# Optimization experiments

Hardware: AMD Instinct MI355X
Metric: run time of the kernel (lower is better)

The kernel has to match this reference:

```python
import math
import jax, jax.numpy as jnp
import numpy as np

B, S, DIM = 1, 2048, 2880
N_HEADS, N_KV, HD = 64, 8, 64
ROPE_FACTOR = 32.0
THETA = 150000.0
NEG_INF = -1e30


def setup_inputs() -> dict:
    key = jax.random.key(0)
    ks = jax.random.split(key, 12)
    std = 0.02
    x = jax.random.normal(ks[0], (B, S, DIM), jnp.float32)
    # rope cache: (S, 2*HD) = [cos | sin], rotate_half convention (angles duplicated)
    inv_freq = 1.0 / (THETA ** (np.arange(0, HD, 2, dtype=np.float32) / HD))
    angles = np.arange(S, dtype=np.float32)[:, None] * inv_freq[None, :]   # (S, HD/2)
    emb = np.concatenate([angles, angles], axis=-1)                        # (S, HD)
    rope_cache = jnp.asarray(np.concatenate([np.cos(emb), np.sin(emb)], axis=-1))  # (S, 2*HD)
    wq_w = jax.random.normal(ks[1], (N_HEADS * HD, DIM), jnp.float32) * std
    wq_b = jax.random.normal(ks[2], (N_HEADS * HD,), jnp.float32) * std
    wk_w = jax.random.normal(ks[3], (N_KV * HD, DIM), jnp.float32) * std
    wk_b = jax.random.normal(ks[4], (N_KV * HD,), jnp.float32) * std
    wv_w = jax.random.normal(ks[5], (N_KV * HD, DIM), jnp.float32) * std
    wv_b = jax.random.normal(ks[6], (N_KV * HD,), jnp.float32) * std
    wo_w = jax.random.normal(ks[7], (DIM, N_HEADS * HD), jnp.float32) * std
    wo_b = jax.random.normal(ks[8], (DIM,), jnp.float32) * std
    sinks = jax.random.normal(ks[9], (N_HEADS,), jnp.float32) * std
    return {"x": x, "rope_cache": rope_cache, "wq_w": wq_w, "wq_b": wq_b,
            "wk_w": wk_w, "wk_b": wk_b, "wv_w": wv_w, "wv_b": wv_b,
            "wo_w": wo_w, "wo_b": wo_b, "sinks": sinks, "sliding_window": 128}


def _rotate_half(t):
    t1, t2 = t[..., : HD // 2], t[..., HD // 2 :]
    return jnp.concatenate([-t2, t1], axis=-1)


def reference(x, rope_cache, wq_w, wq_b, wk_w, wk_b, wv_w, wv_b, wo_w, wo_b, sinks, sliding_window):
    bsz, seqlen, _ = x.shape
    mscale = 0.1 * math.log(ROPE_FACTOR) + 1.0
    scale = mscale / math.sqrt(HD)

    q = (x @ wq_w.T + wq_b).reshape(bsz, seqlen, N_HEADS, HD)
    k = (x @ wk_w.T + wk_b).reshape(bsz, seqlen, N_KV, HD)
    v = (x @ wv_w.T + wv_b).reshape(bsz, seqlen, N_KV, HD)

    cos = rope_cache[:seqlen, :HD][None, :, None, :]   # (1,S,1,HD)
    sin = rope_cache[:seqlen, HD:][None, :, None, :]
    q = q * cos + _rotate_half(q) * sin
    k = k * cos + _rotate_half(k) * sin

    q = q.transpose(0, 2, 1, 3)                        # (B,H,S,hd)
    n_rep = N_HEADS // N_KV
    k = jnp.repeat(k.transpose(0, 2, 1, 3), n_rep, axis=1)  # GQA expand
    v = jnp.repeat(v.transpose(0, 2, 1, 3), n_rep, axis=1)

    scores = jnp.einsum("bhqd,bhkd->bhqk", q, k) * scale
    i = jnp.arange(seqlen)[:, None]
    j = jnp.arange(seqlen)[None, :]
    mask = (j <= i) & ((i - j) < sliding_window)       # causal + sliding window
    scores = jnp.where(mask[None, None], scores, NEG_INF)

    lse = jax.nn.logsumexp(scores, axis=-1)            # (B,H,S)
    attn = jax.nn.softmax(scores, axis=-1)
    out = jnp.einsum("bhqk,bhkd->bhqd", attn, v)

    sink_scale = jax.nn.sigmoid(lse - sinks[None, :, None])[..., None]
    out = out * sink_scale

    out = out.transpose(0, 2, 1, 3).reshape(bsz, seqlen, N_HEADS * HD)
    return out @ wo_w.T + wo_b
```

## Files before the change

### kernel.cpp

```cpp
#include <hip/hip_runtime.h>
#include <hip/hip_bf16.h>
#include <math.h>


typedef __bf16 bf16x8 __attribute__((ext_vector_type(8)));
typedef float  f32x4  __attribute__((ext_vector_type(4)));

#define MFMA_BF16(a,b,c) __builtin_amdgcn_mfma_f32_16x16x32_bf16((a),(b),(c),0,0,0)

__device__ __forceinline__ void gld_lds16(const void* g, void* l) {
    __builtin_amdgcn_global_load_lds(
        (__attribute__((address_space(1))) void*)(g),
        (__attribute__((address_space(3))) void*)(l), 16, 0, 0);
}

__device__ __forceinline__ bf16x8 ld8f(const float* p) {
    f32x4 a = *(const f32x4*)p;
    f32x4 b = *(const f32x4*)(p + 4);
    bf16x8 r;
#pragma unroll
    for (int t = 0; t < 4; t++) { r[t] = (__bf16)a[t]; r[t + 4] = (__bf16)b[t]; }
    return r;
}

__global__ __launch_bounds__(256) void convert_kernel(
    const float* __restrict__ x,  const float* __restrict__ wq,
    const float* __restrict__ wk, const float* __restrict__ wv,
    const float* __restrict__ wo, __bf16* __restrict__ dst)
{
    long e = ((long)blockIdx.x * 256 + threadIdx.x) * 8;
    const float* src; long off;
    if      (e <  5898240L) { src = x;  off = e; }
    else if (e < 17694720L) { src = wq; off = e -  5898240L; }
    else if (e < 19169280L) { src = wk; off = e - 17694720L; }
    else if (e < 20643840L) { src = wv; off = e - 19169280L; }
    else                    { src = wo; off = e - 20643840L; }
    *(bf16x8*)(dst + e) = ld8f(src + off);
}

template <typename TO>
__device__ __forceinline__ void gemm_block(
    const __bf16* __restrict__ A, const __bf16* __restrict__ W,
    const float* __restrict__ bias, TO* __restrict__ C,
    int N, int K, int m0, int n0, __bf16* As, __bf16* Bs)
{
    const int tid  = threadIdx.x;
    const int lane = tid & 63;
    const int wv   = tid >> 6;
    const int wm   = (wv >> 1) * 64;
    const int wn   = (wv & 1) * 64;
    const int quad = lane >> 4;
    const int c    = lane & 15;

    const int arow = tid >> 2;
    const int acol = (tid & 3) * 8;

    int br0 = n0 + arow;      if (br0 > N - 1) br0 = N - 1;
    int br1 = n0 + 64 + arow; if (br1 > N - 1) br1 = N - 1;
    const __bf16* pa0 = A + (size_t)(m0 + arow) * K + acol;
    const __bf16* pa1 = A + (size_t)(m0 + 64 + arow) * K + acol;
    const __bf16* pb0 = W + (size_t)br0 * K + acol;
    const __bf16* pb1 = W + (size_t)br1 * K + acol;

    f32x4 acc[4][4];
#pragma unroll
    for (int i = 0; i < 4; i++)
#pragma unroll
        for (int j = 0; j < 4; j++) acc[i][j] = (f32x4){0.f, 0.f, 0.f, 0.f};

    for (int kk = 0; kk < K; kk += 32) {
        gld_lds16(pa0 + kk, As + tid * 8);
        gld_lds16(pa1 + kk, As + 2048 + tid * 8);
        gld_lds16(pb0 + kk, Bs + tid * 8);
        gld_lds16(pb1 + kk, Bs + 2048 + tid * 8);
        __syncthreads();
        bf16x8 af[4], bfv[4];
#pragma unroll
        for (int i = 0; i < 4; i++)
            af[i] = *(const bf16x8*)&As[(wm + i * 16 + c) * 32 + quad * 8];
#pragma unroll
        for (int j = 0; j < 4; j++)
            bfv[j] = *(const bf16x8*)&Bs[(wn + j * 16 + c) * 32 + quad * 8];
#pragma unroll
        for (int i = 0; i < 4; i++)
#pragma unroll
            for (int j = 0; j < 4; j++)
                acc[i][j] = MFMA_BF16(af[i], bfv[j], acc[i][j]);
        __syncthreads();
    }

#pragma unroll
    for (int j = 0; j < 4; j++) {
        int col = n0 + wn + j * 16 + c;
        if (col >= N) continue;
        float bv = bias[col];
#pragma unroll
        for (int i = 0; i < 4; i++) {
            int row = m0 + wm + i * 16 + quad * 4;
#pragma unroll
            for (int r = 0; r < 4; r++)
                C[(size_t)(row + r) * N + col] = (TO)(acc[i][j][r] + bv);
        }
    }
}

__global__ __launch_bounds__(256) void qkv_kernel(
    const __bf16* __restrict__ x,
    const __bf16* __restrict__ wq, const float* __restrict__ bq,
    const __bf16* __restrict__ wk, const float* __restrict__ bk,
    const __bf16* __restrict__ wv, const float* __restrict__ bv,
    __bf16* __restrict__ qo, __bf16* __restrict__ ko, __bf16* __restrict__ vo)
{
    __shared__ __align__(16) __bf16 As[4096], Bs[4096];
    const int by = blockIdx.y;
    const __bf16 *W; const float* bias; __bf16* C; int N, n0;
    if (by < 32)      { W = wq; bias = bq; C = qo; N = 4096; n0 = by * 128; }
    else if (by < 36) { W = wk; bias = bk; C = ko; N = 512;  n0 = (by - 32) * 128; }
    else              { W = wv; bias = bv; C = vo; N = 512;  n0 = (by - 36) * 128; }
    gemm_block<__bf16>(x, W, bias, C, N, 2880, blockIdx.x * 128, n0, As, Bs);
}

__global__ __launch_bounds__(256) void oproj_kernel(
    const __bf16* __restrict__ a, const __bf16* __restrict__ w,
    const float* __restrict__ b, float* __restrict__ c)
{
    __shared__ __align__(16) __bf16 As[4096], Bs[4096];
    gemm_block<float>(a, w, b, c, 2880, 4096,
                      blockIdx.x * 128, blockIdx.y * 128, As, Bs);
}

__global__ __launch_bounds__(256) void rope_kernel(
    __bf16* __restrict__ qb, __bf16* __restrict__ kb,
    const float* __restrict__ rope)
{
    int idx  = blockIdx.x * 256 + threadIdx.x;
    int dg   = idx & 3;
    int head = (idx >> 2) % 72;
    int s    = (idx >> 2) / 72;
    __bf16* p = (head < 64) ? (qb + (size_t)s * 4096 + head * 64)
                            : (kb + (size_t)s * 512 + (size_t)(head - 64) * 64);
    int d0 = dg * 8;
    bf16x8 x1 = *(bf16x8*)(p + d0);
    bf16x8 x2 = *(bf16x8*)(p + d0 + 32);
    const float* rc = rope + (size_t)s * 128 + d0;
    bf16x8 o1, o2;
#pragma unroll
    for (int t = 0; t < 8; t++) {
        float cc = rc[t], si = rc[64 + t];
        float a = (float)x1[t], b = (float)x2[t];
        o1[t] = (__bf16)(a * cc - b * si);
        o2[t] = (__bf16)(b * cc + a * si);
    }
    *(bf16x8*)(p + d0)      = o1;
    *(bf16x8*)(p + d0 + 32) = o2;
}

__global__ __launch_bounds__(256) void attn_kernel(
    __bf16* __restrict__ q, const __bf16* __restrict__ k,
    const __bf16* __restrict__ v, const float* __restrict__ sinks,
    float  = 0.f)
{
    __shared__ __align__(16) char smem[63488];
    __bf16* Qs = (__bf16*)smem;
    __bf16* Ks = (__bf16*)(smem + 9216);
    __bf16* Vt = (__bf16*)(smem + 36864);
    __bf16* P  = (__bf16*)smem;

    const int tid = threadIdx.x, lane = tid & 63, w = tid >> 6;
    const int quad = lane >> 4, c = lane & 15;
    const int i0 = blockIdx.x * 64;
    const int h  = blockIdx.y;
    const int kvh = h >> 3;
    const int k0 = i0 - 128;

    {
        const int row = tid >> 3;
        const int col = (tid & 7) * 8;
#pragma unroll
        for (int it = 0; it < 2; it++) {
            int r2 = row + it * 32;
            bf16x8 t = *(const bf16x8*)(q + (size_t)(i0 + r2) * 4096 + h * 64 + col);
            *(bf16x8*)&Qs[r2 * 72 + col] = t;
        }
#pragma unroll
        for (int it = 0; it < 6; it++) {
            int r2 = row + it * 32;
            int j = k0 + r2; if (j < 0) j = 0;
            bf16x8 t = *(const bf16x8*)(k + (size_t)j * 512 + kvh * 64 + col);
            *(bf16x8*)&Ks[r2 * 72 + col] = t;
        }
        const int vrow = tid & 31;
        const int d0 = (tid >> 5) * 8;
#pragma unroll
        for (int it = 0; it < 6; it++) {
            int r2 = vrow + it * 32;
            int j = k0 + r2; if (j < 0) j = 0;
            bf16x8 t = *(const bf16x8*)(v + (size_t)j * 512 + kvh * 64 + d0);
#pragma unroll
            for (int u = 0; u < 8; u++) Vt[(d0 + u) * 208 + r2] = t[u];
        }
    }
    __syncthreads();

    f32x4 acc[12];
#pragma unroll
    for (int j = 0; j < 12; j++) acc[j] = (f32x4){0.f, 0.f, 0.f, 0.f};
#pragma unroll
    for (int kt = 0; kt < 2; kt++) {
        bf16x8 af = *(const bf16x8*)&Qs[(w * 16 + c) * 72 + kt * 32 + quad * 8];
#pragma unroll
        for (int j = 0; j < 12; j++) {
            bf16x8 bv = *(const bf16x8*)&Ks[(j * 16 + c) * 72 + kt * 32 + quad * 8];
            acc[j] = MFMA_BF16(af, bv, acc[j]);
        }
    }
    __syncthreads();

    const float scale = 0.16832169878499658f;
    const int igb = i0 + w * 16 + quad * 4;
    float rmax[4] = {-3.0e4f, -3.0e4f, -3.0e4f, -3.0e4f};
#pragma unroll
    for (int j = 0; j < 12; j++) {
        int jg = k0 + j * 16 + c;
#pragma unroll
        for (int r = 0; r < 4; r++) {
            int ig = igb + r;
            bool ok = (jg >= 0) && (jg <= ig) && (ig - jg < 128);
            float vv = ok ? acc[j][r] * scale : -3.0e4f;
            acc[j][r] = vv;
            rmax[r] = fmaxf(rmax[r], vv);
        }
    }
#pragma unroll
    for (int off = 1; off < 16; off <<= 1)
#pragma unroll
        for (int r = 0; r < 4; r++)
            rmax[r] = fmaxf(rmax[r], __shfl_xor(rmax[r], off));

    float rs[4] = {0.f, 0.f, 0.f, 0.f};
#pragma unroll
    for (int j = 0; j < 12; j++)
#pragma unroll
        for (int r = 0; r < 4; r++) {
            float e = __expf(acc[j][r] - rmax[r]);
            acc[j][r] = e;
            rs[r] += e;
        }
#pragma unroll
    for (int off = 1; off < 16; off <<= 1)
#pragma unroll
        for (int r = 0; r < 4; r++)
            rs[r] += __shfl_xor(rs[r], off);

    float rowfac[4];
    {
        float sk = sinks[h];
#pragma unroll
        for (int r = 0; r < 4; r++) {
            float s = fmaxf(rs[r], 1e-20f);
            float lse = rmax[r] + __logf(s);
            rowfac[r] = 1.f / ((1.f + __expf(sk - lse)) * s);
        }
    }

#pragma unroll
    for (int j = 0; j < 12; j++)
#pragma unroll
        for (int r = 0; r < 4; r++)
            P[(w * 16 + quad * 4 + r) * 208 + j * 16 + c] = (__bf16)acc[j][r];
    __syncthreads();

    f32x4 acc2[4];
#pragma unroll
    for (int jd = 0; jd < 4; jd++) acc2[jd] = (f32x4){0.f, 0.f, 0.f, 0.f};
#pragma unroll
    for (int kt = 0; kt < 6; kt++) {
        bf16x8 a = *(const bf16x8*)&P[(w * 16 + c) * 208 + kt * 32 + quad * 8];
#pragma unroll
        for (int jd = 0; jd < 4; jd++) {
            bf16x8 b = *(const bf16x8*)&Vt[(jd * 16 + c) * 208 + kt * 32 + quad * 8];
            acc2[jd] = MFMA_BF16(a, b, acc2[jd]);
        }
    }
#pragma unroll
    for (int jd = 0; jd < 4; jd++)
#pragma unroll
        for (int r = 0; r < 4; r++) {
            int qr = w * 16 + quad * 4 + r;
            q[(size_t)(i0 + qr) * 4096 + h * 64 + jd * 16 + c] =
                (__bf16)(acc2[jd][r] * rowfac[r]);
        }
}

extern "C" void kernel_launch(void* const* d_in, const int* in_sizes, int n_in,
                              void* d_out, int out_size, void* d_ws, size_t ws_size,
                              hipStream_t stream) {
    const float* x    = (const float*)d_in[0];
    const float* rope = (const float*)d_in[1];
    const float* wq   = (const float*)d_in[2];
    const float* bq   = (const float*)d_in[3];
    const float* wk   = (const float*)d_in[4];
    const float* bk   = (const float*)d_in[5];
    const float* wv   = (const float*)d_in[6];
    const float* bv   = (const float*)d_in[7];
    const float* wo   = (const float*)d_in[8];
    const float* bo   = (const float*)d_in[9];
    const float* sk   = (const float*)d_in[10];
    float* out = (float*)d_out;

    __bf16* wsb = (__bf16*)d_ws;
    __bf16* xb  = wsb;
    __bf16* wqb = wsb +  5898240L;
    __bf16* wkb = wsb + 17694720L;
    __bf16* wvb = wsb + 19169280L;
    __bf16* wob = wsb + 20643840L;
    __bf16* qb  = wsb + 32440320L;
    __bf16* kb  = wsb + 40828928L;
    __bf16* vb  = wsb + 41877504L;

    convert_kernel<<<15840, 256, 0, stream>>>(x, wq, wk, wv, wo, xb);
    qkv_kernel<<<dim3(16, 40), 256, 0, stream>>>(xb, wqb, bq, wkb, bk, wvb, bv,
                                                 qb, kb, vb);
    rope_kernel<<<2304, 256, 0, stream>>>(qb, kb, rope);
    attn_kernel<<<dim3(32, 64), 256, 0, stream>>>(qb, kb, vb, sk);
    oproj_kernel<<<dim3(16, 23), 256, 0, stream>>>(qb, wob, bo, out);
}
```

Baseline: 409.3 us.

## Split-K the output projection and deepen GEMM K-step to 64

```diff
diff --git a/kernel.cpp b/kernel.cpp
--- a/kernel.cpp
+++ b/kernel.cpp
@@ -39,10 +39,11 @@
 }
 
 template <typename TO>
-__device__ __forceinline__ void gemm_block(
+__device__ __forceinline__ void gemm_block64(
     const __bf16* __restrict__ A, const __bf16* __restrict__ W,
     const float* __restrict__ bias, TO* __restrict__ C,
-    int N, int K, int m0, int n0, __bf16* As, __bf16* Bs)
+    int N, int Ks, int kBeg, int kEnd, int m0, int n0,
+    __bf16* As, __bf16* Bs)
 {
     const int tid  = threadIdx.x;
     const int lane = tid & 63;
@@ -52,15 +53,15 @@
     const int quad = lane >> 4;
     const int c    = lane & 15;
 
-    const int arow = tid >> 2;
-    const int acol = (tid & 3) * 8;
-
-    int br0 = n0 + arow;      if (br0 > N - 1) br0 = N - 1;
-    int br1 = n0 + 64 + arow; if (br1 > N - 1) br1 = N - 1;
-    const __bf16* pa0 = A + (size_t)(m0 + arow) * K + acol;
-    const __bf16* pa1 = A + (size_t)(m0 + 64 + arow) * K + acol;
-    const __bf16* pb0 = W + (size_t)br0 * K + acol;
-    const __bf16* pb1 = W + (size_t)br1 * K + acol;
+    const int srow = tid >> 2;
+    const int scol = (tid & 3) * 8;
+
+    int br0 = n0 + srow;      if (br0 > N - 1) br0 = N - 1;
+    int br1 = n0 + 64 + srow; if (br1 > N - 1) br1 = N - 1;
+    const __bf16* pa0 = A + (size_t)(m0 + srow) * Ks + scol;
+    const __bf16* pa1 = A + (size_t)(m0 + 64 + srow) * Ks + scol;
+    const __bf16* pb0 = W + (size_t)br0 * Ks + scol;
+    const __bf16* pb1 = W + (size_t)br1 * Ks + scol;
 
     f32x4 acc[4][4];
 #pragma unroll
@@ -68,24 +69,30 @@
 #pragma unroll
         for (int j = 0; j < 4; j++) acc[i][j] = (f32x4){0.f, 0.f, 0.f, 0.f};
 
-    for (int kk = 0; kk < K; kk += 32) {
-        gld_lds16(pa0 + kk, As + tid * 8);
-        gld_lds16(pa1 + kk, As + 2048 + tid * 8);
-        gld_lds16(pb0 + kk, Bs + tid * 8);
-        gld_lds16(pb1 + kk, Bs + 2048 + tid * 8);
+    for (int kk = kBeg; kk < kEnd; kk += 64) {
+        gld_lds16(pa0 + kk,      As + tid * 8);
+        gld_lds16(pa1 + kk,      As + 2048 + tid * 8);
+        gld_lds16(pa0 + kk + 32, As + 4096 + tid * 8);
+        gld_lds16(pa1 + kk + 32, As + 6144 + tid * 8);
+        gld_lds16(pb0 + kk,      Bs + tid * 8);
+        gld_lds16(pb1 + kk,      Bs + 2048 + tid * 8);
+        gld_lds16(pb0 + kk + 32, Bs + 4096 + tid * 8);
+        gld_lds16(pb1 + kk + 32, Bs + 6144 + tid * 8);
         __syncthreads();
-        bf16x8 af[4], bfv[4];
-#pragma unroll
-        for (int i = 0; i < 4; i++)
-            af[i] = *(const bf16x8*)&As[(wm + i * 16 + c) * 32 + quad * 8];
-#pragma unroll
-        for (int j = 0; j < 4; j++)
-            bfv[j] = *(const bf16x8*)&Bs[(wn + j * 16 + c) * 32 + quad * 8];
-#pragma unroll
-        for (int i = 0; i < 4; i++)
+        for (int kt = 0; kt < 2; kt++) {
+            bf16x8 af[4], bfv[4];
+#pragma unroll
+            for (int i = 0; i < 4; i++)
+                af[i] = *(const bf16x8*)&As[kt * 4096 + (wm + i * 16 + c) * 32 + quad * 8];
 #pragma unroll
             for (int j = 0; j < 4; j++)
-                acc[i][j] = MFMA_BF16(af[i], bfv[j], acc[i][j]);
+                bfv[j] = *(const bf16x8*)&Bs[kt * 4096 + (wn + j * 16 + c) * 32 + quad * 8];
+#pragma unroll
+            for (int i = 0; i < 4; i++)
+#pragma unroll
+                for (int j = 0; j < 4; j++)
+                    acc[i][j] = MFMA_BF16(af[i], bfv[j], acc[i][j]);
+        }
         __syncthreads();
     }
 
@@ -93,7 +100,7 @@
     for (int j = 0; j < 4; j++) {
         int col = n0 + wn + j * 16 + c;
         if (col >= N) continue;
-        float bv = bias[col];
+        float bv = bias ? bias[col] : 0.0f;
 #pragma unroll
         for (int i = 0; i < 4; i++) {
             int row = m0 + wm + i * 16 + quad * 4;
@@ -104,29 +111,50 @@
     }
 }
 
-__global__ __launch_bounds__(256) void qkv_kernel(
+__global__ __launch_bounds__(256, 3) void qkv_kernel(
     const __bf16* __restrict__ x,
     const __bf16* __restrict__ wq, const float* __restrict__ bq,
     const __bf16* __restrict__ wk, const float* __restrict__ bk,
     const __bf16* __restrict__ wv, const float* __restrict__ bv,
     __bf16* __restrict__ qo, __bf16* __restrict__ ko, __bf16* __restrict__ vo)
 {
-    __shared__ __align__(16) __bf16 As[4096], Bs[4096];
+    __shared__ __align__(16) __bf16 As[8192], Bs[8192];
     const int by = blockIdx.y;
     const __bf16 *W; const float* bias; __bf16* C; int N, n0;
     if (by < 32)      { W = wq; bias = bq; C = qo; N = 4096; n0 = by * 128; }
     else if (by < 36) { W = wk; bias = bk; C = ko; N = 512;  n0 = (by - 32) * 128; }
     else              { W = wv; bias = bv; C = vo; N = 512;  n0 = (by - 36) * 128; }
-    gemm_block<__bf16>(x, W, bias, C, N, 2880, blockIdx.x * 128, n0, As, Bs);
-}
-
-__global__ __launch_bounds__(256) void oproj_kernel(
+    gemm_block64<__bf16>(x, W, bias, C, N, 2880, 0, 2880,
+                         blockIdx.x * 128, n0, As, Bs);
+}
+
+__global__ __launch_bounds__(256, 3) void oproj_kernel(
     const __bf16* __restrict__ a, const __bf16* __restrict__ w,
-    const float* __restrict__ b, float* __restrict__ c)
-{
-    __shared__ __align__(16) __bf16 As[4096], Bs[4096];
-    gemm_block<float>(a, w, b, c, 2880, 4096,
-                      blockIdx.x * 128, blockIdx.y * 128, As, Bs);
+    __bf16* __restrict__ p0, __bf16* __restrict__ p1)
+{
+    __shared__ __align__(16) __bf16 As[8192], Bs[8192];
+    const int z = blockIdx.z;
+    __bf16* C = z ? p1 : p0;
+    gemm_block64<__bf16>(a, w, nullptr, C, 2880, 4096, z * 2048, (z + 1) * 2048,
+                         blockIdx.x * 128, blockIdx.y * 128, As, Bs);
+}
+
+__global__ __launch_bounds__(256) void reduce_kernel(
+    const __bf16* __restrict__ p0, const __bf16* __restrict__ p1,
+    const float* __restrict__ bo, float* __restrict__ out)
+{
+    long e = ((long)blockIdx.x * 256 + threadIdx.x) * 8;
+    int col = (int)(e % 2880L);
+    bf16x8 a = *(const bf16x8*)(p0 + e);
+    bf16x8 b = *(const bf16x8*)(p1 + e);
+    f32x4 o0, o1;
+#pragma unroll
+    for (int t = 0; t < 4; t++) {
+        o0[t] = (float)a[t]     + (float)b[t]     + bo[col + t];
+        o1[t] = (float)a[4 + t] + (float)b[4 + t] + bo[col + 4 + t];
+    }
+    *(f32x4*)(out + e)     = o0;
+    *(f32x4*)(out + e + 4) = o1;
 }
 
 __global__ __launch_bounds__(256) void rope_kernel(
@@ -157,8 +185,7 @@
 
 __global__ __launch_bounds__(256) void attn_kernel(
     __bf16* __restrict__ q, const __bf16* __restrict__ k,
-    const __bf16* __restrict__ v, const float* __restrict__ sinks,
-    float  = 0.f)
+    const __bf16* __restrict__ v, const float* __restrict__ sinks)
 {
     __shared__ __align__(16) char smem[63488];
     __bf16* Qs = (__bf16*)smem;
@@ -317,11 +344,14 @@
     __bf16* qb  = wsb + 32440320L;
     __bf16* kb  = wsb + 40828928L;
     __bf16* vb  = wsb + 41877504L;
+    __bf16* p0  = wsb;
+    __bf16* p1  = wsb +  5898240L;
 
     convert_kernel<<<15840, 256, 0, stream>>>(x, wq, wk, wv, wo, xb);
     qkv_kernel<<<dim3(16, 40), 256, 0, stream>>>(xb, wqb, bq, wkb, bk, wvb, bv,
                                                  qb, kb, vb);
     rope_kernel<<<2304, 256, 0, stream>>>(qb, kb, rope);
     attn_kernel<<<dim3(32, 64), 256, 0, stream>>>(qb, kb, vb, sk);
-    oproj_kernel<<<dim3(16, 23), 256, 0, stream>>>(qb, wob, bo, out);
-}
+    oproj_kernel<<<dim3(16, 23, 2), 256, 0, stream>>>(qb, wob, p0, p1);
+    reduce_kernel<<<2880, 256, 0, stream>>>(p0, p1, bo, out);
+}
```

Measured after the change: 349.3 us. 14.6% less time.
